# Performance work log

Hardware: AMD Instinct MI355X
Metric: run time of the kernel (lower is better)

## Reference

```python
import jax, jax.numpy as jnp
import numpy as np

B, T, D = 8, 1024, 512
V = 8192  # codebook_size


def setup_inputs() -> dict:
    key = jax.random.key(0)
    k1, k2, k3 = jax.random.split(key, 3)
    scale_w = float(np.sqrt(2.0 / (D + V)))  # xavier_uniform-ish scale
    scale_c = float(np.sqrt(2.0 / (V + D)))
    return {
        "inputs": jax.random.normal(k1, (B, T, D), dtype=jnp.float32),
        "codebook": jax.random.normal(k2, (V, D), dtype=jnp.float32) * scale_c,
        "W_logits": jax.random.normal(k3, (V, D), dtype=jnp.float32) * scale_w,
        "b_logits": jnp.zeros((V,), dtype=jnp.float32),
    }


def reference(inputs, codebook, W_logits, b_logits):
    # logits = Linear(input_dim -> codebook_size)
    logits = jnp.einsum("btd,vd->btv", inputs, W_logits) + b_logits  # [B,T,V]
    # eval mode: no gumbel noise, no temperature division
    soft_tokens = jax.nn.softmax(logits, axis=-1)
    token_indices = jnp.argmax(soft_tokens, axis=-1)  # [B,T]
    hard_tokens = jax.nn.one_hot(token_indices, codebook.shape[0], dtype=soft_tokens.dtype)
    # straight-through: hard values, soft gradients
    tokens_for_lookup = soft_tokens + jax.lax.stop_gradient(hard_tokens - soft_tokens)
    quantized = jnp.einsum("btv,vd->btd", tokens_for_lookup, codebook)  # [B,T,D]
    commitment_loss = jnp.mean((quantized - jax.lax.stop_gradient(inputs)) ** 2)
    return quantized, token_indices, commitment_loss, soft_tokens, logits
```

## Files before the change

kernel.cpp:

```cpp
#include <hip/hip_runtime.h>
#include <hip/hip_bf16.h>

#define BT_ 8192
#define D_  512
#define V_  8192

#define NCHUNK 4
#define CROWS  2048

#define OFF_Q      0
#define OFF_TOK    4194304
#define OFF_LOSS   4202496
#define OFF_SOFT   4202497
#define OFF_LOGITS 71311361
#define STAGE_F    62922752

#define TAU  0.02f

typedef __attribute__((ext_vector_type(8))) short bf16x8;
typedef __attribute__((ext_vector_type(4))) float f32x4;
typedef __attribute__((ext_vector_type(4))) unsigned short u16x4;

__device__ __forceinline__ unsigned short bf16rne(float f) {
  unsigned int u = __float_as_uint(f);
  return (unsigned short)((u + 0x7fffu + ((u >> 16) & 1u)) >> 16);
}

__global__ __launch_bounds__(256) void to_bf16_k(const f32x4* __restrict__ x,
                                                 const f32x4* __restrict__ w,
                                                 u16x4* __restrict__ xa,
                                                 u16x4* __restrict__ wb) {
  const int n4 = (BT_ * D_) / 4;
  const int half = gridDim.x >> 1;
  const bool isw = blockIdx.x >= half;
  const f32x4* __restrict__ s = isw ? w : x;
  u16x4* __restrict__ d = isw ? wb : xa;
  const int b0 = isw ? blockIdx.x - half : blockIdx.x;
  for (int i = b0 * 256 + threadIdx.x; i < n4; i += half * 256) {
    const f32x4 v = s[i];
    u16x4 o;
    o[0] = bf16rne(v[0]); o[1] = bf16rne(v[1]);
    o[2] = bf16rne(v[2]); o[3] = bf16rne(v[3]);
    d[i] = o;
  }
}

__device__ __forceinline__ void gload_lds16(const void* g, void* l) {
  __builtin_amdgcn_global_load_lds((const __attribute__((address_space(1))) void*)g,
                                   (__attribute__((address_space(3))) void*)l,
                                   16, 0, 0);
}

__device__ __forceinline__ void barf() {
  __builtin_amdgcn_s_barrier();
  asm volatile("" ::: "memory");
}
__device__ __forceinline__ void vmcnt2() { asm volatile("s_waitcnt vmcnt(2)" ::: "memory"); }
__device__ __forceinline__ void vmcnt0() { asm volatile("s_waitcnt vmcnt(0)" ::: "memory"); }

__device__ __forceinline__ void stage_unit(const char* __restrict__ tb, char* ldsRegion,
                                           int ktile, int half, int wid, int lane) {
#pragma unroll
  for (int issue = 0; issue < 2; ++issue) {
    const int d = half * 16384 + issue * 8192 + wid * 1024 + lane * 16;
    const int l = d ^ (((d >> 7) & 7) << 4);
    gload_lds16(tb + (size_t)(l >> 7) * 1024 + ktile * 128 + (l & 127),
                ldsRegion + half * 16384 + issue * 8192 + wid * 1024);
  }
}

__device__ __forceinline__ bf16x8 rdfrag(const char* base, int R, int ks, int g) {
  return *(const bf16x8*)(base + R * 128 + ((ks * 64 + 16 * g) ^ ((R & 7) << 4)));
}

__device__ __forceinline__ void kgroup(int t, int smode, char* lds,
                                       const char* __restrict__ Ab,
                                       const char* __restrict__ Bb,
                                       int wr, int wc, int lane, int wid,
                                       f32x4 (&acc)[8][4]) {
  char* aL = lds + (t & 1) * 32768;
  char* bL = lds + 65536 + (t & 1) * 32768;
  char* aS = lds + ((t & 1) ^ 1) * 32768;
  char* bS = lds + 65536 + ((t & 1) ^ 1) * 32768;
  const int cg = lane & 15, g = lane >> 4;
  bf16x8 a[4][2], b0[2][2], b1[2][2];

#pragma unroll
  for (int m = 0; m < 4; ++m)
#pragma unroll
    for (int ks = 0; ks < 2; ++ks)
      a[m][ks] = rdfrag(aL, wr * 128 + m * 16 + cg, ks, g);
#pragma unroll
  for (int n = 0; n < 2; ++n)
#pragma unroll
    for (int ks = 0; ks < 2; ++ks)
      b0[n][ks] = rdfrag(bL, wc * 64 + n * 16 + cg, ks, g);
  if (smode >= 1) stage_unit(Ab, aS, t + 1, 1, wid, lane);
  barf();
  __builtin_amdgcn_s_setprio(1);
#pragma unroll
  for (int m = 0; m < 4; ++m)
#pragma unroll
    for (int n = 0; n < 2; ++n)
#pragma unroll
      for (int ks = 0; ks < 2; ++ks)
        acc[m][n] = __builtin_amdgcn_mfma_f32_16x16x32_bf16(a[m][ks], b0[n][ks], acc[m][n], 0, 0, 0);
  __builtin_amdgcn_s_setprio(0);
  barf();

#pragma unroll
  for (int n = 0; n < 2; ++n)
#pragma unroll
    for (int ks = 0; ks < 2; ++ks)
      b1[n][ks] = rdfrag(bL, wc * 64 + (n + 2) * 16 + cg, ks, g);
  if (smode >= 1) stage_unit(Bb, bS, t + 1, 0, wid, lane);
  barf();
  __builtin_amdgcn_s_setprio(1);
#pragma unroll
  for (int m = 0; m < 4; ++m)
#pragma unroll
    for (int n = 0; n < 2; ++n)
#pragma unroll
      for (int ks = 0; ks < 2; ++ks)
        acc[m][n + 2] = __builtin_amdgcn_mfma_f32_16x16x32_bf16(a[m][ks], b1[n][ks], acc[m][n + 2], 0, 0, 0);
  __builtin_amdgcn_s_setprio(0);
  barf();

#pragma unroll
  for (int m = 0; m < 4; ++m)
#pragma unroll
    for (int ks = 0; ks < 2; ++ks)
      a[m][ks] = rdfrag(aL, wr * 128 + (m + 4) * 16 + cg, ks, g);
  if (smode >= 1) stage_unit(Bb, bS, t + 1, 1, wid, lane);
  barf();
  __builtin_amdgcn_s_setprio(1);
#pragma unroll
  for (int m = 0; m < 4; ++m)
#pragma unroll
    for (int n = 0; n < 2; ++n)
#pragma unroll
      for (int ks = 0; ks < 2; ++ks)
        acc[m + 4][n + 2] = __builtin_amdgcn_mfma_f32_16x16x32_bf16(a[m][ks], b1[n][ks], acc[m + 4][n + 2], 0, 0, 0);
  __builtin_amdgcn_s_setprio(0);
  barf();

  if (smode == 2) stage_unit(Ab, aL, t + 2, 0, wid, lane);
  barf();
  __builtin_amdgcn_s_setprio(1);
#pragma unroll
  for (int m = 0; m < 4; ++m)
#pragma unroll
    for (int n = 0; n < 2; ++n)
#pragma unroll
      for (int ks = 0; ks < 2; ++ks)
        acc[m + 4][n] = __builtin_amdgcn_mfma_f32_16x16x32_bf16(a[m][ks], b0[n][ks], acc[m + 4][n], 0, 0, 0);
  __builtin_amdgcn_s_setprio(0);
  if (smode == 2) vmcnt2();
  else if (smode == 1) vmcnt0();
  barf();
}

__global__ __launch_bounds__(512) void gemm8(const unsigned short* __restrict__ A,
                                             const unsigned short* __restrict__ B,
                                             const float* __restrict__ bias,
                                             float* __restrict__ C,
                                             float* __restrict__ pmaxT,
                                             float* __restrict__ psumT,
                                             int rowBase) {
  __shared__ char lds[131072];
  const int tid  = threadIdx.x;
  const int lane = tid & 63;
  const int wid  = tid >> 6;
  const int wr   = wid >> 2, wc = wid & 3;

  const int bid = blockIdx.x;
  const int by  = bid & 7;
  const int bx  = bid >> 3;
  const int row0 = rowBase + by * 256;
  const int col0 = bx * 256;

  const char* Ab = (const char*)A + (size_t)row0 * (D_ * 2);
  const char* Bb = (const char*)B + (size_t)col0 * (D_ * 2);

  f32x4 acc[8][4] = {};

  stage_unit(Ab, lds, 0, 0, wid, lane);
  stage_unit(Ab, lds, 0, 1, wid, lane);
  stage_unit(Bb, lds + 65536, 0, 0, wid, lane);
  stage_unit(Bb, lds + 65536, 0, 1, wid, lane);
  stage_unit(Ab, lds + 32768, 1, 0, wid, lane);
  vmcnt2();
  barf();

  for (int t = 0; t < 6; ++t)
    kgroup(t, 2, lds, Ab, Bb, wr, wc, lane, wid, acc);
  kgroup(6, 1, lds, Ab, Bb, wr, wc, lane, wid, acc);
  kgroup(7, 0, lds, Ab, Bb, wr, wc, lane, wid, acc);

  const int cg = lane & 15, g = lane >> 4;
  float bv[4];
#pragma unroll
  for (int n = 0; n < 4; ++n) bv[n] = bias[col0 + wc * 64 + n * 16 + cg];

  float* cl = (float*)lds;
  __syncthreads();
#pragma unroll
  for (int h = 0; h < 2; ++h) {
    if (wr == h) {
#pragma unroll
      for (int m = 0; m < 8; ++m)
#pragma unroll
        for (int n = 0; n < 4; ++n) {
          const int cw = ((wc * 64 + n * 16 + cg) + 253) & 255;
#pragma unroll
          for (int rr = 0; rr < 4; ++rr) {
            const int R = m * 16 + 4 * g + rr;
            cl[R * 256 + cw] = acc[m][n][rr] + bv[n];
          }
        }
    }
    __syncthreads();
#pragma unroll
    for (int k = 0; k < 16; ++k) {
      const int r = wid * 16 + k;
      const f32x4 v = *(const f32x4*)((char*)cl + r * 1024 + lane * 16);
      float vmx = fmaxf(fmaxf(v[0], v[1]), fmaxf(v[2], v[3]));
      float vsm = __expf(v[0]) + __expf(v[1]) + __expf(v[2]) + __expf(v[3]);
#pragma unroll
      for (int o = 1; o < 64; o <<= 1) {
        vmx = fmaxf(vmx, __shfl_xor(vmx, o));
        vsm += __shfl_xor(vsm, o);
      }
      const int grow = row0 + h * 128 + r;
      float* Crow = C + (size_t)grow * V_ + col0;
      if (lane < 63) {
        *((f32x4*)(Crow + 3) + lane) = v;
      } else {
        Crow[255] = v[0]; Crow[0] = v[1]; Crow[1] = v[2]; Crow[2] = v[3];
      }
      if (lane == 0) {
        pmaxT[(size_t)bx * BT_ + grow] = vmx;
        psumT[(size_t)bx * BT_ + grow] = vsm;
      }
    }
    __syncthreads();
  }
}

__global__ __launch_bounds__(256) void row_finish(const float* __restrict__ logits,
                                                  const float* __restrict__ pmaxT,
                                                  const float* __restrict__ psumT,
                                                  const float* __restrict__ xf,
                                                  const float* __restrict__ wf,
                                                  const float* __restrict__ bias,
                                                  float* __restrict__ tokf,
                                                  float* __restrict__ soft,
                                                  int rowBase) {
  const int row  = rowBase + blockIdx.x;
  const int tid  = threadIdx.x;
  const int lane = tid & 63;
  const int wv   = tid >> 6;

  const int tl = lane & 31;
  const float pm = pmaxT[(size_t)tl * BT_ + row];
  const float ps = psumT[(size_t)tl * BT_ + row];
  float m = pm, s = ps;
#pragma unroll
  for (int o = 1; o < 32; o <<= 1) {
    m = fmaxf(m, __shfl_xor(m, o));
    s += __shfl_xor(s, o);
  }
  const float si = 1.0f / s;

  const float* L = logits + (size_t)row * V_;
  float*       S = soft   + (size_t)row * V_;
  const f32x4* L4 = (const f32x4*)(L + 3);
  f32x4*       S4 = (f32x4*)(S + 3);

  if (wv == 0) {
    const float thr = m - TAU;
    unsigned long long tmask = __ballot(pm >= thr) & 0xFFFFFFFFull;
    float bestv = -1e30f;
    int   besti = 0x7fffffff;
    const float4* xr4 = (const float4*)(xf + (size_t)row * D_);
    while (tmask) {
      const int t = __ffsll(tmask) - 1;
      tmask &= tmask - 1;
      const float* Lr = L + t * 256;
#pragma unroll
      for (int kq = 0; kq < 4; ++kq) {
        const float lv = Lr[kq * 64 + lane];
        unsigned long long c = __ballot(lv >= thr);
        while (c) {
          const int j = __ffsll(c) - 1;
          c &= c - 1;
          const int col = t * 256 + kq * 64 + j;
          const float4* wr4 = (const float4*)(wf + (size_t)col * D_);
          float p = 0.f;
#pragma unroll
          for (int q = 0; q < 2; ++q) {
            const float4 av = xr4[lane + 64 * q];
            const float4 bvv = wr4[lane + 64 * q];
            p += av.x * bvv.x + av.y * bvv.y + av.z * bvv.z + av.w * bvv.w;
          }
#pragma unroll
          for (int o = 1; o < 64; o <<= 1) p += __shfl_xor(p, o);
          const float tot = p + bias[col];
          if (tot > bestv || (tot == bestv && col < besti)) { bestv = tot; besti = col; }
        }
      }
    }
    if (lane == 0) tokf[row] = (float)besti;
    if (lane < 3)  S[lane] = __expf(L[lane]) * si;
    if (lane == 3) S[8191] = __expf(L[8191]) * si;
#pragma unroll
    for (int k = 0; k < 2; ++k) {
      const int i = 1920 + k * 64 + lane;
      if (i < 2047) {
        const f32x4 v = L4[i];
        f32x4 o;
        o[0] = __expf(v[0]) * si; o[1] = __expf(v[1]) * si;
        o[2] = __expf(v[2]) * si; o[3] = __expf(v[3]) * si;
        __builtin_nontemporal_store(o, S4 + i);
      }
    }
  } else {
    const int t = tid - 64;
#pragma unroll
    for (int k = 0; k < 10; ++k) {
      const int i = k * 192 + t;
      const f32x4 v = L4[i];
      f32x4 o;
      o[0] = __expf(v[0]) * si; o[1] = __expf(v[1]) * si;
      o[2] = __expf(v[2]) * si; o[3] = __expf(v[3]) * si;
      __builtin_nontemporal_store(o, S4 + i);
    }
  }
}

__global__ __launch_bounds__(256) void finalize_k(const float* __restrict__ tokf,
                                                  const float* __restrict__ cb,
                                                  const float* __restrict__ xf,
                                                  float* __restrict__ q,
                                                  float* __restrict__ loss) {
  const int row  = blockIdx.x * 4 + (threadIdx.x >> 6);
  const int lane = threadIdx.x & 63;
  const int idx  = (int)tokf[row];
  const f32x4* cr = (const f32x4*)(cb + (size_t)idx * D_);
  const f32x4* xr = (const f32x4*)(xf + (size_t)row * D_);
  f32x4* qr = (f32x4*)(q + (size_t)row * D_);
  float ls = 0.f;
#pragma unroll
  for (int j = 0; j < 2; ++j) {
    const int c = lane + j * 64;
    const f32x4 cv = cr[c];
    const f32x4 xv = xr[c];
    __builtin_nontemporal_store(cv, qr + c);
    const float dx = cv[0] - xv[0], dy = cv[1] - xv[1], dz = cv[2] - xv[2], dw = cv[3] - xv[3];
    ls += dx * dx + dy * dy + dz * dz + dw * dw;
  }
#pragma unroll
  for (int o = 32; o; o >>= 1) ls += __shfl_xor(ls, o);
  if (lane == 0) atomicAdd(loss, ls * (1.0f / 4194304.0f));
}

extern "C" void kernel_launch(void* const* d_in, const int* in_sizes, int n_in,
                              void* d_out, int out_size, void* d_ws, size_t ws_size,
                              hipStream_t stream) {
  const float* x  = (const float*)d_in[0];
  const float* cb = (const float*)d_in[1];
  const float* wl = (const float*)d_in[2];
  const float* bl = (const float*)d_in[3];
  float* out = (float*)d_out;

  float* qout   = out + OFF_Q;
  float* tokf   = out + OFF_TOK;
  float* loss   = out + OFF_LOSS;
  float* soft   = out + OFF_SOFT;
  float* logits = out + OFF_LOGITS;

  unsigned short* Abf = (unsigned short*)(out + STAGE_F);
  unsigned short* Wbf = Abf + (size_t)BT_ * D_;
  float* pmaxT = qout;
  float* psumT = qout + 262144;

  hipMemsetAsync(loss, 0, 4, stream);

  to_bf16_k<<<2048, 256, 0, stream>>>((const f32x4*)x, (const f32x4*)wl,
                                      (u16x4*)Abf, (u16x4*)Wbf);
  for (int c = 0; c < NCHUNK; ++c) {
    gemm8<<<256, 512, 0, stream>>>(Abf, Wbf, bl, logits, pmaxT, psumT, c * CROWS);
    row_finish<<<CROWS, 256, 0, stream>>>(logits, pmaxT, psumT, x, wl, bl,
                                          tokf, soft, c * CROWS);
  }
  finalize_k<<<2048, 256, 0, stream>>>(tokf, cb, x, qout, loss);
}
```

Before: 380.9 us.

## Move softmax stats into row_finish and run GEMM as one XCD-aware launch

The GEMM epilogue no longer computes per-tile max/sum partials. row_finish now reads each logits row once, keeps the exponentials in registers, reduces max and sum across the block, and collects argmax candidates into shared memory with atomics before rescoring them in fp32. The four chunked GEMM and row_finish launches become one GEMM launch, with blocks remapped so each XCD gets a contiguous 2D tile region, and one row_finish launch. This trades chunk-level overlap and the cheaper partial-stat path for fewer launches and less global traffic. The candidate list is capped at 64, which risks missing the true argmax if a row has many near-ties.

```diff
diff --git a/kernel.cpp b/kernel.cpp
--- a/kernel.cpp
+++ b/kernel.cpp
@@ -4,9 +4,6 @@
 #define BT_ 8192
 #define D_  512
 #define V_  8192
-
-#define NCHUNK 4
-#define CROWS  2048
 
 #define OFF_Q      0
 #define OFF_TOK    4194304
@@ -16,6 +13,8 @@
 #define STAGE_F    62922752
 
 #define TAU  0.02f
+#define EXP_NEG_TAU 0.98019867f
+#define MAXC 64
 
 typedef __attribute__((ext_vector_type(8))) short bf16x8;
 typedef __attribute__((ext_vector_type(4))) float f32x4;
@@ -163,10 +162,7 @@
 __global__ __launch_bounds__(512) void gemm8(const unsigned short* __restrict__ A,
                                              const unsigned short* __restrict__ B,
                                              const float* __restrict__ bias,
-                                             float* __restrict__ C,
-                                             float* __restrict__ pmaxT,
-                                             float* __restrict__ psumT,
-                                             int rowBase) {
+                                             float* __restrict__ C) {
   __shared__ char lds[131072];
   const int tid  = threadIdx.x;
   const int lane = tid & 63;
@@ -174,10 +170,11 @@
   const int wr   = wid >> 2, wc = wid & 3;
 
   const int bid = blockIdx.x;
-  const int by  = bid & 7;
-  const int bx  = bid >> 3;
-  const int row0 = rowBase + by * 256;
-  const int col0 = bx * 256;
+  const int xcd = bid & 7;
+  const int s   = bid >> 3;
+  const int by  = (xcd >> 1) * 8 + (s >> 4);
+  const int bx  = (xcd & 1) * 16 + (s & 15);
+  const int row0 = by * 256, col0 = bx * 256;
 
   const char* Ab = (const char*)A + (size_t)row0 * (D_ * 2);
   const char* Bb = (const char*)B + (size_t)col0 * (D_ * 2);
@@ -224,13 +221,6 @@
     for (int k = 0; k < 16; ++k) {
       const int r = wid * 16 + k;
       const f32x4 v = *(const f32x4*)((char*)cl + r * 1024 + lane * 16);
-      float vmx = fmaxf(fmaxf(v[0], v[1]), fmaxf(v[2], v[3]));
-      float vsm = __expf(v[0]) + __expf(v[1]) + __expf(v[2]) + __expf(v[3]);
-#pragma unroll
-      for (int o = 1; o < 64; o <<= 1) {
-        vmx = fmaxf(vmx, __shfl_xor(vmx, o));
-        vsm += __shfl_xor(vsm, o);
-      }
       const int grow = row0 + h * 128 + r;
       float* Crow = C + (size_t)grow * V_ + col0;
       if (lane < 63) {
@@ -238,104 +228,120 @@
       } else {
         Crow[255] = v[0]; Crow[0] = v[1]; Crow[1] = v[2]; Crow[2] = v[3];
       }
-      if (lane == 0) {
-        pmaxT[(size_t)bx * BT_ + grow] = vmx;
-        psumT[(size_t)bx * BT_ + grow] = vsm;
-      }
     }
     __syncthreads();
   }
 }
 
 __global__ __launch_bounds__(256) void row_finish(const float* __restrict__ logits,
-                                                  const float* __restrict__ pmaxT,
-                                                  const float* __restrict__ psumT,
                                                   const float* __restrict__ xf,
                                                   const float* __restrict__ wf,
                                                   const float* __restrict__ bias,
                                                   float* __restrict__ tokf,
-                                                  float* __restrict__ soft,
-                                                  int rowBase) {
-  const int row  = rowBase + blockIdx.x;
+                                                  float* __restrict__ soft) {
+  const int row  = blockIdx.x;
   const int tid  = threadIdx.x;
   const int lane = tid & 63;
   const int wv   = tid >> 6;
 
-  const int tl = lane & 31;
-  const float pm = pmaxT[(size_t)tl * BT_ + row];
-  const float ps = psumT[(size_t)tl * BT_ + row];
-  float m = pm, s = ps;
-#pragma unroll
-  for (int o = 1; o < 32; o <<= 1) {
-    m = fmaxf(m, __shfl_xor(m, o));
-    s += __shfl_xor(s, o);
-  }
-  const float si = 1.0f / s;
+  __shared__ float redM[4], redS[4];
+  __shared__ int   cnum;
+  __shared__ int   cidx[MAXC];
 
   const float* L = logits + (size_t)row * V_;
   float*       S = soft   + (size_t)row * V_;
   const f32x4* L4 = (const f32x4*)(L + 3);
   f32x4*       S4 = (f32x4*)(S + 3);
 
+  f32x4 e[8];
+  float m_e = 0.f, s = 0.f;
+#pragma unroll
+  for (int j = 0; j < 8; ++j) {
+    const int i = j * 256 + tid;
+    if (i < 2047) {
+      const f32x4 v = L4[i];
+      f32x4 t;
+      t[0] = __expf(v[0]); t[1] = __expf(v[1]);
+      t[2] = __expf(v[2]); t[3] = __expf(v[3]);
+      e[j] = t;
+      m_e = fmaxf(m_e, fmaxf(fmaxf(t[0], t[1]), fmaxf(t[2], t[3])));
+      s += t[0] + t[1] + t[2] + t[3];
+    } else {
+      e[j][0] = 0.f; e[j][1] = 0.f; e[j][2] = 0.f; e[j][3] = 0.f;
+    }
+  }
+  float extra_e = 0.f;
+  int   extra_col = -1;
+  if (tid < 3)       extra_col = tid;
+  else if (tid == 3) extra_col = 8191;
+  if (extra_col >= 0) {
+    extra_e = __expf(L[extra_col]);
+    m_e = fmaxf(m_e, extra_e);
+    s += extra_e;
+  }
+#pragma unroll
+  for (int o = 1; o < 64; o <<= 1) {
+    m_e = fmaxf(m_e, __shfl_xor(m_e, o));
+    s += __shfl_xor(s, o);
+  }
+  if (lane == 0) { redM[wv] = m_e; redS[wv] = s; }
+  if (tid == 0) cnum = 0;
+  __syncthreads();
+  m_e = fmaxf(fmaxf(redM[0], redM[1]), fmaxf(redM[2], redM[3]));
+  s   = redS[0] + redS[1] + redS[2] + redS[3];
+  const float si    = 1.0f / s;
+  const float thr_e = m_e * EXP_NEG_TAU;
+
+#pragma unroll
+  for (int j = 0; j < 8; ++j) {
+    const int i = j * 256 + tid;
+#pragma unroll
+    for (int q = 0; q < 4; ++q)
+      if (e[j][q] >= thr_e) {
+        const int p = atomicAdd(&cnum, 1);
+        if (p < MAXC) cidx[p] = 3 + 4 * i + q;
+      }
+  }
+  if (extra_col >= 0 && extra_e >= thr_e) {
+    const int p = atomicAdd(&cnum, 1);
+    if (p < MAXC) cidx[p] = extra_col;
+  }
+  __syncthreads();
+
   if (wv == 0) {
-    const float thr = m - TAU;
-    unsigned long long tmask = __ballot(pm >= thr) & 0xFFFFFFFFull;
+    const int cnt = min(cnum, MAXC);
     float bestv = -1e30f;
     int   besti = 0x7fffffff;
     const float4* xr4 = (const float4*)(xf + (size_t)row * D_);
-    while (tmask) {
-      const int t = __ffsll(tmask) - 1;
-      tmask &= tmask - 1;
-      const float* Lr = L + t * 256;
-#pragma unroll
-      for (int kq = 0; kq < 4; ++kq) {
-        const float lv = Lr[kq * 64 + lane];
-        unsigned long long c = __ballot(lv >= thr);
-        while (c) {
-          const int j = __ffsll(c) - 1;
-          c &= c - 1;
-          const int col = t * 256 + kq * 64 + j;
-          const float4* wr4 = (const float4*)(wf + (size_t)col * D_);
-          float p = 0.f;
-#pragma unroll
-          for (int q = 0; q < 2; ++q) {
-            const float4 av = xr4[lane + 64 * q];
-            const float4 bvv = wr4[lane + 64 * q];
-            p += av.x * bvv.x + av.y * bvv.y + av.z * bvv.z + av.w * bvv.w;
-          }
-#pragma unroll
-          for (int o = 1; o < 64; o <<= 1) p += __shfl_xor(p, o);
-          const float tot = p + bias[col];
-          if (tot > bestv || (tot == bestv && col < besti)) { bestv = tot; besti = col; }
-        }
+    for (int c = 0; c < cnt; ++c) {
+      const int col = cidx[c];
+      const float4* wr4 = (const float4*)(wf + (size_t)col * D_);
+      float p = 0.f;
+#pragma unroll
+      for (int q = 0; q < 2; ++q) {
+        const float4 av = xr4[lane + 64 * q];
+        const float4 bvv = wr4[lane + 64 * q];
+        p += av.x * bvv.x + av.y * bvv.y + av.z * bvv.z + av.w * bvv.w;
       }
+#pragma unroll
+      for (int o = 1; o < 64; o <<= 1) p += __shfl_xor(p, o);
+      const float tot = p + bias[col];
+      if (tot > bestv || (tot == bestv && col < besti)) { bestv = tot; besti = col; }
     }
     if (lane == 0) tokf[row] = (float)besti;
-    if (lane < 3)  S[lane] = __expf(L[lane]) * si;
-    if (lane == 3) S[8191] = __expf(L[8191]) * si;
-#pragma unroll
-    for (int k = 0; k < 2; ++k) {
-      const int i = 1920 + k * 64 + lane;
-      if (i < 2047) {
-        const f32x4 v = L4[i];
-        f32x4 o;
-        o[0] = __expf(v[0]) * si; o[1] = __expf(v[1]) * si;
-        o[2] = __expf(v[2]) * si; o[3] = __expf(v[3]) * si;
-        __builtin_nontemporal_store(o, S4 + i);
-      }
-    }
-  } else {
-    const int t = tid - 64;
-#pragma unroll
-    for (int k = 0; k < 10; ++k) {
-      const int i = k * 192 + t;
-      const f32x4 v = L4[i];
+  }
+
+#pragma unroll
+  for (int j = 0; j < 8; ++j) {
+    const int i = j * 256 + tid;
+    if (i < 2047) {
       f32x4 o;
-      o[0] = __expf(v[0]) * si; o[1] = __expf(v[1]) * si;
-      o[2] = __expf(v[2]) * si; o[3] = __expf(v[3]) * si;
+      o[0] = e[j][0] * si; o[1] = e[j][1] * si;
+      o[2] = e[j][2] * si; o[3] = e[j][3] * si;
       __builtin_nontemporal_store(o, S4 + i);
     }
   }
+  if (extra_col >= 0) S[extra_col] = extra_e * si;
 }
 
 __global__ __launch_bounds__(256) void finalize_k(const float* __restrict__ tokf,
@@ -381,17 +387,12 @@
 
   unsigned short* Abf = (unsigned short*)(out + STAGE_F);
   unsigned short* Wbf = Abf + (size_t)BT_ * D_;
-  float* pmaxT = qout;
-  float* psumT = qout + 262144;
 
   hipMemsetAsync(loss, 0, 4, stream);
 
   to_bf16_k<<<2048, 256, 0, stream>>>((const f32x4*)x, (const f32x4*)wl,
                                       (u16x4*)Abf, (u16x4*)Wbf);
-  for (int c = 0; c < NCHUNK; ++c) {
-    gemm8<<<256, 512, 0, stream>>>(Abf, Wbf, bl, logits, pmaxT, psumT, c * CROWS);
-    row_finish<<<CROWS, 256, 0, stream>>>(logits, pmaxT, psumT, x, wl, bl,
-                                          tokf, soft, c * CROWS);
-  }
+  gemm8<<<1024, 512, 0, stream>>>(Abf, Wbf, bl, logits);
+  row_finish<<<8192, 256, 0, stream>>>(logits, x, wl, bl, tokf, soft);
   finalize_k<<<2048, 256, 0, stream>>>(tokf, cb, x, qout, loss);
 }
```

Measured after the change: 335.2 us. -12.0%, faster.
